# Kernel optimization log

Measured on AMD Instinct MI355X. Metric: run time of the kernel, lower is better.

Reference implementation:

```python
import jax, jax.numpy as jnp
import numpy as np

LEADER_IDX = 0
SOCIAL_DIST = 1.5
COHESION = 0.8
B, N, T = 64, 64, 100


def setup_inputs() -> dict:
    key = jax.random.key(0)
    k1, k2, k3, k4, k5 = jax.random.split(key, 5)
    # trajectories: (x, y, vel, yaw, acc, yawvel)
    x = jax.random.normal(k1, (B, N, T, 6), dtype=jnp.float32) * 5.0
    # world_from_agent: per-agent SE(2) homogeneous transform (B, 3, 3)
    theta = jax.random.uniform(k2, (B,), minval=-np.pi, maxval=np.pi)
    c, s = jnp.cos(theta), jnp.sin(theta)
    trans = jax.random.normal(k3, (B, 2), dtype=jnp.float32) * 50.0
    wfa = (jnp.zeros((B, 3, 3), dtype=jnp.float32)
           .at[:, 0, 0].set(c).at[:, 0, 1].set(-s)
           .at[:, 1, 0].set(s).at[:, 1, 1].set(c)
           .at[:, :2, 2].set(trans).at[:, 2, 2].set(1.0))
    # externalized randomness of torch forward (randint over B-1 choices, rand<p)
    rand_idx = jax.random.randint(k4, (T * N, B), 0, B - 1, dtype=jnp.int32)
    drop_mask = jax.random.uniform(k5, (T * N, B)) < COHESION
    return {"x": x, "world_from_agent": wfa, "rand_idx": rand_idx, "drop_mask": drop_mask}


def reference(x, world_from_agent, rand_idx, drop_mask):
    pos = x[..., :2]                                   # (B, N, T, 2)
    R = world_from_agent[:, :2, :2]                    # (B, 2, 2)
    t = world_from_agent[:, :2, 2]                     # (B, 2)
    pos_g = jnp.einsum('bntj,bij->bnti', pos, R) + t[:, None, None, :]
    # leader positions are detached (no grad), but same value in fwd
    leader = (jnp.arange(B) == LEADER_IDX)[:, None, None, None]
    pos_g = jnp.where(leader, jax.lax.stop_gradient(pos_g), pos_g)
    # (B,N,T,2) -> (T,N,B,2) -> (T*N, B, 2)  (matches torch transpose(0,2).reshape)
    flat = jnp.transpose(pos_g, (2, 1, 0, 3)).reshape(T * N, B, 2)
    # pairwise euclidean distances via norm trick (avoids (TN,B,B,2) diff tensor)
    sq = jnp.sum(flat * flat, axis=-1)                 # (TN, B)
    d2 = sq[:, :, None] + sq[:, None, :] - 2.0 * jnp.einsum('tbd,tcd->tbc', flat, flat)
    dist = jnp.sqrt(jnp.maximum(d2, 1e-12))            # (TN, B, B)
    eye = jnp.eye(B, dtype=bool)
    dist = jnp.where(eye[None], jnp.inf, dist)         # mask self-distance
    min_nb = jnp.argmin(dist, axis=-1).astype(jnp.int32)      # (TN, B)
    # row b of neighbor_choices is [0..b-1, b+1..B-1]; gather at rand_idx ->
    # value = rand_idx + (rand_idx >= b)
    b_idx = jnp.arange(B, dtype=jnp.int32)[None, :]
    rand_nb = rand_idx + (rand_idx >= b_idx).astype(jnp.int32)
    nb = jnp.where(drop_mask, rand_nb, min_nb)         # (TN, B)
    nd = jnp.take_along_axis(dist, nb[..., None], axis=2)[..., 0]  # (TN, B)
    nd = jnp.transpose(nd.reshape(T, N, B), (2, 1, 0))  # (B, N, T)
    loss = jnp.mean((nd - SOCIAL_DIST) ** 2, axis=-1)   # (B, N)
    return loss
```

## Files before the change

kernel.cpp:

```cpp
#include <hip/hip_runtime.h>

#define BB 64
#define NN 64
#define TT 100
#define TQ 4
#define NTQ (TT / TQ)

__device__ __forceinline__ float bcast(float v, int lane) {
    return __int_as_float(__builtin_amdgcn_readlane(__float_as_int(v), lane));
}

__global__ __launch_bounds__(256) void social_slice_kernel(
    const float* __restrict__ x,
    const float* __restrict__ wfa,
    const int* __restrict__ rand_idx,
    const int* __restrict__ drop_mask,
    float* __restrict__ ws)
{
    const int n  = blockIdx.x & 63;
    const int tq = blockIdx.x >> 6;
    const int t0 = tq * TQ;

    __shared__ float2 S[TQ][BB + 1];
    __shared__ float  Rld[TQ][BB];

    {
        const int lb = threadIdx.x >> 2;
        const int k  = threadIdx.x & 3;
        const float* wp = wfa + lb * 9;
        const float r00 = wp[0], r01 = wp[1], tx = wp[2];
        const float r10 = wp[3], r11 = wp[4], ty = wp[5];
        const size_t xoff = (((size_t)lb * NN + n) * (size_t)TT + (size_t)(t0 + k)) * 6;
        const float2 p = *(const float2*)(x + xoff);
        const float gx = r00 * p.x + r01 * p.y + tx;
        const float gy = r10 * p.x + r11 * p.y + ty;
        S[k][lb] = make_float2(gx, gy);
    }
    __syncthreads();

    const int w = threadIdx.x >> 6;
    const int b = threadIdx.x & 63;
    const int t = t0 + w;
    const int s = t * NN + n;
    const size_t sb = (size_t)s * BB + b;
    const int r  = rand_idx[sb];
    const int dm = drop_mask[sb];

    const float2 g = S[w][b];
    const float gx = g.x, gy = g.y;
    const float sq = gx * gx + gy * gy;

    float bd0 = 3.4e38f, bd1 = 3.4e38f, bd2 = 3.4e38f, bd3 = 3.4e38f;
    int   bi0 = 0, bi1 = 16, bi2 = 32, bi3 = 48;
    #pragma unroll
    for (int i = 0; i < 16; ++i) {
        {
            const int c = i;
            const float qx = bcast(gx, c), qy = bcast(gy, c), qz = bcast(sq, c);
            float d2 = fmaf(-2.0f, fmaf(gx, qx, gy * qy), sq + qz);
            d2 = fmaxf(d2, 1e-12f);
            const bool take = (c != b) && (d2 < bd0);
            bd0 = take ? d2 : bd0;  bi0 = take ? c : bi0;
        }
        {
            const int c = 16 + i;
            const float qx = bcast(gx, c), qy = bcast(gy, c), qz = bcast(sq, c);
            float d2 = fmaf(-2.0f, fmaf(gx, qx, gy * qy), sq + qz);
            d2 = fmaxf(d2, 1e-12f);
            const bool take = (c != b) && (d2 < bd1);
            bd1 = take ? d2 : bd1;  bi1 = take ? c : bi1;
        }
        {
            const int c = 32 + i;
            const float qx = bcast(gx, c), qy = bcast(gy, c), qz = bcast(sq, c);
            float d2 = fmaf(-2.0f, fmaf(gx, qx, gy * qy), sq + qz);
            d2 = fmaxf(d2, 1e-12f);
            const bool take = (c != b) && (d2 < bd2);
            bd2 = take ? d2 : bd2;  bi2 = take ? c : bi2;
        }
        {
            const int c = 48 + i;
            const float qx = bcast(gx, c), qy = bcast(gy, c), qz = bcast(sq, c);
            float d2 = fmaf(-2.0f, fmaf(gx, qx, gy * qy), sq + qz);
            d2 = fmaxf(d2, 1e-12f);
            const bool take = (c != b) && (d2 < bd3);
            bd3 = take ? d2 : bd3;  bi3 = take ? c : bi3;
        }
    }
    float best = bd0; int besti = bi0;
    if (bd1 < best) { best = bd1; besti = bi1; }
    if (bd2 < best) { best = bd2; besti = bi2; }
    if (bd3 < best) { best = bd3; besti = bi3; }

    const int rnb = r + (r >= b ? 1 : 0);
    const int nb  = dm ? rnb : besti;

    const float qx = __shfl(gx, nb);
    const float qy = __shfl(gy, nb);
    const float qz = __shfl(sq, nb);
    const float dot = fmaf(gx, qx, gy * qy);
    const float d2m = fmaxf(fmaf(-2.0f, dot, sq + qz), 1e-12f);
    const float nd = sqrtf(d2m);
    const float diff = nd - 1.5f;
    Rld[w][b] = diff * diff;
    __syncthreads();

    if (w == 0) {
        const float sum4 = ((Rld[0][b] + Rld[1][b]) + Rld[2][b]) + Rld[3][b];
        ws[((size_t)tq * NN + n) * BB + b] = sum4;
    }
}

__global__ __launch_bounds__(256) void social_reduce_kernel(
    const float* __restrict__ ws,
    float* __restrict__ out)
{
    const int b = threadIdx.x & 63;
    const int n = blockIdx.x * 4 + (threadIdx.x >> 6);

    float acc = 0.f;
    #pragma unroll
    for (int tq = 0; tq < NTQ; ++tq)
        acc += ws[((size_t)tq * NN + n) * BB + b];
    out[b * NN + n] = acc * (1.0f / TT);
}

extern "C" void kernel_launch(void* const* d_in, const int* in_sizes, int n_in,
                              void* d_out, int out_size, void* d_ws, size_t ws_size,
                              hipStream_t stream) {
    const float* x = (const float*)d_in[0];
    const float* wfa = (const float*)d_in[1];
    const int* rand_idx = (const int*)d_in[2];
    const int* drop_mask = (const int*)d_in[3];
    float* out = (float*)d_out;
    float* ws = (float*)d_ws;

    social_slice_kernel<<<NTQ * NN, 256, 0, stream>>>(
        x, wfa, rand_idx, drop_mask, ws);
    social_reduce_kernel<<<NN / 4, 256, 0, stream>>>(ws, out);
}
```

Before: 76.52 us.

## Fuse reduction into slice kernel via last-block atomic counter

Replaces the separate reduction kernel with a last-block-done pattern. Each block publishes its partial sums, bumps a per-agent atomic counter, and the block that finishes last for that agent sums all time-chunk partials and writes the output. This is meant to remove a second kernel launch and its dependency gap. In exchange it adds a memset launch for the counters, fences and atomics, and a serial tail in the last block.

```diff
diff --git a/kernel.cpp b/kernel.cpp
--- a/kernel.cpp
+++ b/kernel.cpp
@@ -5,17 +5,20 @@
 #define TT 100
 #define TQ 4
 #define NTQ (TT / TQ)
+#define CNT_OFF (NTQ * NN * BB)
 
 __device__ __forceinline__ float bcast(float v, int lane) {
     return __int_as_float(__builtin_amdgcn_readlane(__float_as_int(v), lane));
 }
 
-__global__ __launch_bounds__(256) void social_slice_kernel(
+__global__ __launch_bounds__(256) void social_fused_kernel(
     const float* __restrict__ x,
     const float* __restrict__ wfa,
     const int* __restrict__ rand_idx,
     const int* __restrict__ drop_mask,
-    float* __restrict__ ws)
+    float* __restrict__ ws,
+    unsigned* __restrict__ cnt,
+    float* __restrict__ out)
 {
     const int n  = blockIdx.x & 63;
     const int tq = blockIdx.x >> 6;
@@ -23,6 +26,7 @@
 
     __shared__ float2 S[TQ][BB + 1];
     __shared__ float  Rld[TQ][BB];
+    __shared__ int    islast;
 
     {
         const int lb = threadIdx.x >> 2;
@@ -107,22 +111,28 @@
 
     if (w == 0) {
         const float sum4 = ((Rld[0][b] + Rld[1][b]) + Rld[2][b]) + Rld[3][b];
-        ws[((size_t)tq * NN + n) * BB + b] = sum4;
+        __hip_atomic_store(&ws[((size_t)tq * NN + n) * BB + b], sum4,
+                           __ATOMIC_RELAXED, __HIP_MEMORY_SCOPE_AGENT);
+        __threadfence();
+        if (b == 0) {
+            const unsigned old = __hip_atomic_fetch_add(
+                &cnt[n], 1u, __ATOMIC_ACQ_REL, __HIP_MEMORY_SCOPE_AGENT);
+            islast = (old == NTQ - 1) ? 1 : 0;
+        }
     }
-}
+    __syncthreads();
+    if (!islast) return;
 
-__global__ __launch_bounds__(256) void social_reduce_kernel(
-    const float* __restrict__ ws,
-    float* __restrict__ out)
-{
-    const int b = threadIdx.x & 63;
-    const int n = blockIdx.x * 4 + (threadIdx.x >> 6);
-
+    __threadfence();
     float acc = 0.f;
-    #pragma unroll
-    for (int tq = 0; tq < NTQ; ++tq)
-        acc += ws[((size_t)tq * NN + n) * BB + b];
-    out[b * NN + n] = acc * (1.0f / TT);
+    for (int tqq = w; tqq < NTQ; tqq += TQ)
+        acc += __hip_atomic_load(&ws[((size_t)tqq * NN + n) * BB + b],
+                                 __ATOMIC_RELAXED, __HIP_MEMORY_SCOPE_AGENT);
+    __syncthreads();
+    Rld[w][b] = acc;
+    __syncthreads();
+    if (w == 0)
+        out[b * NN + n] = (((Rld[0][b] + Rld[1][b]) + Rld[2][b]) + Rld[3][b]) * (1.0f / TT);
 }
 
 extern "C" void kernel_launch(void* const* d_in, const int* in_sizes, int n_in,
@@ -134,8 +144,10 @@
     const int* drop_mask = (const int*)d_in[3];
     float* out = (float*)d_out;
     float* ws = (float*)d_ws;
+    unsigned* cnt = (unsigned*)((char*)d_ws + CNT_OFF * sizeof(float));
 
-    social_slice_kernel<<<NTQ * NN, 256, 0, stream>>>(
-        x, wfa, rand_idx, drop_mask, ws);
-    social_reduce_kernel<<<NN / 4, 256, 0, stream>>>(ws, out);
+    hipMemsetAsync(cnt, 0, NN * sizeof(unsigned), stream);
+
+    social_fused_kernel<<<NTQ * NN, 256, 0, stream>>>(
+        x, wfa, rand_idx, drop_mask, ws, cnt, out);
 }
```

Measured after the change: 123.5 us. +61.4%, slower.
